# Performance work log

Hardware: AMD Instinct MI355X
Metric: run time of the kernel (lower is better)

Reference implementation:

```python
import jax, jax.numpy as jnp
import numpy as np

VOCAB = 32000
HID = 1024


def _gru_cell(Wih, Whh, bih, bhh, h, x):
    # PyTorch GRU gate order: r, z, n
    gx = Wih @ x + bih          # [3H]
    gh = Whh @ h + bhh          # [3H]
    H = h.shape[0]
    r = jax.nn.sigmoid(gx[:H] + gh[:H])
    z = jax.nn.sigmoid(gx[H:2 * H] + gh[H:2 * H])
    n = jnp.tanh(gx[2 * H:] + r * gh[2 * H:])
    return (1.0 - z) * n + z * h


def setup_inputs() -> dict:
    key = jax.random.key(0)
    ks = jax.random.split(key, 13)
    S = 512
    T = 512
    s = 1.0 / np.sqrt(HID)
    u = lambda k, shape: jax.random.uniform(k, shape, jnp.float32, -s, s)
    return {
        "inputs": jax.random.randint(ks[0], (S,), 0, VOCAB, jnp.int32),
        "targets": jax.random.randint(ks[1], (T,), 0, VOCAB, jnp.int32),
        "emb": jax.random.normal(ks[2], (VOCAB, HID), jnp.float32),
        "enc_Wih": u(ks[3], (3 * HID, HID)),
        "enc_Whh": u(ks[4], (3 * HID, HID)),
        "enc_bih": u(ks[5], (3 * HID,)),
        "enc_bhh": u(ks[6], (3 * HID,)),
        "dec_Wih": u(ks[7], (3 * HID, HID)),
        "dec_Whh": u(ks[8], (3 * HID, HID)),
        "dec_bih": u(ks[9], (3 * HID,)),
        "dec_bhh": u(ks[10], (3 * HID,)),
        "proj_W": u(ks[11], (VOCAB, HID)),
        "proj_b": u(ks[12], (VOCAB,)),
    }


def reference(inputs, targets, emb, enc_Wih, enc_Whh, enc_bih, enc_bhh,
              dec_Wih, dec_Whh, dec_bih, dec_bhh, proj_W, proj_b):
    # Encoder: scan GRU over embedded source tokens (batch=1, state [H])
    src_emb = emb[inputs]  # [S,H]
    h0 = jnp.zeros((HID,), src_emb.dtype)

    def enc_step(h, x):
        return _gru_cell(enc_Wih, enc_Whh, enc_bih, enc_bhh, h, x), None

    enc_state, _ = jax.lax.scan(enc_step, h0, src_emb)

    # Decoder: teacher forcing; input token at step i is 0 (start) then targets[i-1]
    dec_tokens = jnp.concatenate([jnp.zeros((1,), targets.dtype), targets[:-1]])
    dec_emb = emb[dec_tokens]  # [T,H]

    def dec_step(h, x):
        h_new = _gru_cell(dec_Wih, dec_Whh, dec_bih, dec_bhh, h, x)
        return h_new, h_new

    _, dec_hs = jax.lax.scan(dec_step, enc_state, dec_emb)  # [T,H]

    # Projection to vocab logits (single GEMM over all timesteps)
    logits = dec_hs @ proj_W.T + proj_b  # [T,V]
    return logits
```

## Files before the change

### kernel.cpp

```cpp
#include <hip/hip_runtime.h>
#include <cstdint>
#include <cstddef>

#define H 1024
#define SEQ 512
#define THREEH 3072
#define VOCABN 32000
#define NBLK 64
#define NWORK 192
#define HPB 16

#define HBIAS 2.0f
#define HVALID 0.5f

template <int CTRL>
__device__ __forceinline__ float dpp_add(float v) {
    return v + __int_as_float(__builtin_amdgcn_update_dpp(
        0, __float_as_int(v), CTRL, 0xF, 0xF, true));
}
__device__ __forceinline__ float row16_sum(float v) {
    v = dpp_add<0xB1>(v);
    v = dpp_add<0x4E>(v);
    v = dpp_add<0x124>(v);
    v = dpp_add<0x128>(v);
    return v;
}

__device__ void rnn_path(int blk, int tid, float* smem,
    const float* __restrict__ eWhh, const float* __restrict__ ebhh,
    const float* __restrict__ dWhh, const float* __restrict__ dbhh,
    const float* __restrict__ gxe, const float* __restrict__ gxd,
    float* __restrict__ enc_t, float* __restrict__ dec_t)
{
    const int wave = tid >> 6;
    const int lane = tid & 63;
    const int g = lane >> 4;
    const int p = lane & 15;
    const int i0 = blk * HPB;
    const int myidx = i0 + 4 * wave + g;

    float* hs0 = smem;
    float* hs1 = smem + H;

    float4 wreg[3][16];
    float br, bz, bn;
    float hown = 0.f;

    auto load_w = [&](const float* __restrict__ W, const float* __restrict__ b) {
        float ws[3];
#pragma unroll
        for (int gate = 0; gate < 3; ++gate) {
            const float* base = W + (size_t)(gate * H + myidx) * H + 64 * p;
            float s = 0.f;
#pragma unroll
            for (int k = 0; k < 16; ++k) {
                float4 w = *(const float4*)(base + 4 * ((k + p) & 15));
                wreg[gate][k] = w;
                s += w.x + w.y + w.z + w.w;
            }
            ws[gate] = s;
        }
        br = b[myidx]         - HBIAS * row16_sum(ws[0]);
        bz = b[H + myidx]     - HBIAS * row16_sum(ws[1]);
        bn = b[2 * H + myidx] - HBIAS * row16_sum(ws[2]);
    };

    load_w(eWhh, ebhh);

    for (int step = 0; step < 2 * SEQ; ++step) {
        const bool dec = step >= SEQ;
        const int t = dec ? step - SEQ : step;
        if (dec && t == 0) load_w(dWhh, dbhh);

        const float* gx = dec ? gxd : gxe;
        float* tb_out = (dec ? dec_t : enc_t) + (size_t)t * H;
        float* hb = (step & 1) ? hs1 : hs0;

        const float* gxp = gx + (size_t)t * THREEH + myidx;
        float gxr = gxp[0];
        float gxz = gxp[H];
        float gxn = gxp[2 * H];

        if (step == 0) {
            *(float4*)&hb[wave * 256 + lane * 4] =
                float4{HBIAS, HBIAS, HBIAS, HBIAS};
        } else {
            const float* tb_prev =
                (step <= SEQ) ? enc_t + (size_t)(step - 1) * H
                              : dec_t + (size_t)(step - SEQ - 1) * H;
            const unsigned long long* src =
                (const unsigned long long*)tb_prev + wave * 128 + lane * 2;
            union { unsigned long long u; float f[2]; } cv[2];
            for (;;) {
                cv[0].u = __hip_atomic_load(src,
                    __ATOMIC_RELAXED, __HIP_MEMORY_SCOPE_AGENT);
                cv[1].u = __hip_atomic_load(src + 1,
                    __ATOMIC_RELAXED, __HIP_MEMORY_SCOPE_AGENT);
                if ((cv[0].f[0] > HVALID) & (cv[0].f[1] > HVALID) &
                    (cv[1].f[0] > HVALID) & (cv[1].f[1] > HVALID)) break;
                __builtin_amdgcn_s_sleep(1);
            }
            *(float4*)&hb[wave * 256 + lane * 4] =
                float4{cv[0].f[0], cv[0].f[1], cv[1].f[0], cv[1].f[1]};
        }
        __syncthreads();

        float a0 = 0.f, a1 = 0.f, a2 = 0.f;
#pragma unroll
        for (int k = 0; k < 16; ++k) {
            float4 h = *(const float4*)&hb[64 * p + 4 * ((k + p) & 15)];
            float4 w0 = wreg[0][k], w1 = wreg[1][k], w2 = wreg[2][k];
            a0 += w0.x * h.x + w0.y * h.y + w0.z * h.z + w0.w * h.w;
            a1 += w1.x * h.x + w1.y * h.y + w1.z * h.z + w1.w * h.w;
            a2 += w2.x * h.x + w2.y * h.y + w2.z * h.z + w2.w * h.w;
        }
        float sr = row16_sum(a0);
        float sz = row16_sum(a1);
        float sn = row16_sum(a2);

        float rg = 1.f / (1.f + expf(-(gxr + sr + br)));
        float zg = 1.f / (1.f + expf(-(gxz + sz + bz)));
        float ng = tanhf(gxn + rg * (sn + bn));
        float hnew = (1.f - zg) * ng + zg * hown;
        hown = hnew;

        if (p == 0)
            __hip_atomic_store(tb_out + myidx, hnew + HBIAS,
                               __ATOMIC_RELAXED, __HIP_MEMORY_SCOPE_AGENT);
    }
}

template <int MODE>
__device__ void gemm_tile(const float* __restrict__ Abase,
                          int m0, int n0,
                          const float* __restrict__ W,
                          const float* __restrict__ bias,
                          float* __restrict__ C, int N,
                          float* __restrict__ sA, float* __restrict__ sB)
{
    const int tid = threadIdx.x;
    const int r = tid >> 2;
    const int c = tid & 3;
    const int tx = tid & 15;
    const int ty = tid >> 4;
    const int m = m0 + r;

    const float* Arow = Abase + (size_t)m * H;
    const float* Brow = W + (size_t)(n0 + r) * H;
    const float abias = (MODE == 2) ? HBIAS : 0.f;

    float acc[4][4] = {};
    for (int k0 = 0; k0 < H; k0 += 16) {
        float4 av = *(const float4*)(Arow + k0 + c * 4);
        float4 bv = *(const float4*)(Brow + k0 + c * 4);
        __syncthreads();
        sA[(c * 4 + 0) * 68 + r] = av.x - abias;
        sA[(c * 4 + 1) * 68 + r] = av.y - abias;
        sA[(c * 4 + 2) * 68 + r] = av.z - abias;
        sA[(c * 4 + 3) * 68 + r] = av.w - abias;
        sB[(c * 4 + 0) * 68 + r] = bv.x;
        sB[(c * 4 + 1) * 68 + r] = bv.y;
        sB[(c * 4 + 2) * 68 + r] = bv.z;
        sB[(c * 4 + 3) * 68 + r] = bv.w;
        __syncthreads();
#pragma unroll
        for (int kk = 0; kk < 16; ++kk) {
            float4 a = *(const float4*)&sA[kk * 68 + ty * 4];
            float4 b = *(const float4*)&sB[kk * 68 + tx * 4];
            float avv[4] = {a.x, a.y, a.z, a.w};
            float bvv[4] = {b.x, b.y, b.z, b.w};
#pragma unroll
            for (int i = 0; i < 4; ++i)
#pragma unroll
                for (int jj = 0; jj < 4; ++jj)
                    acc[i][jj] += avv[i] * bvv[jj];
        }
    }
    float4 bq = *(const float4*)(bias + n0 + tx * 4);
    float bb[4] = {bq.x, bq.y, bq.z, bq.w};
#pragma unroll
    for (int i = 0; i < 4; ++i) {
        float4 o;
        o.x = acc[i][0] + bb[0];
        o.y = acc[i][1] + bb[1];
        o.z = acc[i][2] + bb[2];
        o.w = acc[i][3] + bb[3];
        *(float4*)&C[(size_t)(m0 + ty * 4 + i) * N + n0 + tx * 4] = o;
    }
}

__device__ void worker_path(int wid, int tid, float* smem,
    const float* __restrict__ dec_t,
    const float* __restrict__ pW, const float* __restrict__ pb,
    float* __restrict__ out)
{
    float* sA = smem;
    float* sB = smem + 16 * 68;

    {
        float acc = 0.f;
        const size_t nlines = (size_t)VOCABN * H / 32;
        for (size_t i = (size_t)wid * 256 + tid; i < nlines;
             i += (size_t)NWORK * 256)
            acc += pW[i * 32];
        asm volatile("" :: "v"(acc));
    }

    int cur = -1;
    for (int tt = wid; tt < 8 * 500; tt += NWORK) {
        int mb = tt / 500, nb = tt % 500;
        if (mb != cur) {
            if (tid < 64) {
                const unsigned long long* src =
                    (const unsigned long long*)(dec_t + (size_t)(mb * 64 + 63) * H);
                for (;;) {
                    bool ok = true;
#pragma unroll
                    for (int m = 0; m < 8; ++m) {
                        union { unsigned long long u; float f[2]; } c;
                        c.u = __hip_atomic_load(src + tid + 64 * m,
                            __ATOMIC_RELAXED, __HIP_MEMORY_SCOPE_AGENT);
                        ok &= (c.f[0] > HVALID) & (c.f[1] > HVALID);
                    }
                    if (ok) break;
                    __builtin_amdgcn_s_sleep(64);
                }
            }
            __syncthreads();
            __builtin_amdgcn_fence(__ATOMIC_ACQUIRE, "agent");
            cur = mb;
        }
        gemm_tile<2>(dec_t, mb * 64, nb * 64, pW, pb, out, VOCABN, sA, sB);
    }
}

__global__ __launch_bounds__(256, 1) void fused_rnn(
    const float* __restrict__ eWhh, const float* __restrict__ ebhh,
    const float* __restrict__ dWhh, const float* __restrict__ dbhh,
    const float* __restrict__ gxe, const float* __restrict__ gxd,
    float* __restrict__ enc_t, float* __restrict__ dec_t,
    const float* __restrict__ pW, const float* __restrict__ pb,
    float* __restrict__ out)
{
    __shared__ float smem[2176];
    const int b = blockIdx.x;
    if (b < NBLK)
        rnn_path(b, threadIdx.x, smem, eWhh, ebhh, dWhh, dbhh,
                 gxe, gxd, enc_t, dec_t);
    else
        worker_path(b - NBLK, threadIdx.x, smem, dec_t, pW, pb, out);
}

__global__ __launch_bounds__(256, 2) void gemm_nt(
    const float* __restrict__ Abase,
    const int* __restrict__ toks0,
    const int* __restrict__ toks1,
    const int mode,
    const float* __restrict__ W,
    const float* __restrict__ bias,
    float* __restrict__ C, const int N)
{
    constexpr int TM = 64, TN = 64, TK = 16;
    __shared__ float As[TK][TM + 4];
    __shared__ float Bs[TK][TN + 4];
    const int tid = threadIdx.x;
    const int n0 = blockIdx.x * TN;
    const int m0 = blockIdx.y * TM;
    const int r = tid >> 2;
    const int c = tid & 3;
    const int tx = tid & 15;
    const int ty = tid >> 4;

    const int m = m0 + r;
    const float* Arow;
    if (mode == 0) Arow = Abase + (size_t)toks0[m] * H;
    else           Arow = Abase + (size_t)(m == 0 ? 0 : toks1[m - 1]) * H;
    const float* Brow = W + (size_t)(n0 + r) * H;

    float acc[4][4] = {};
    for (int k0 = 0; k0 < H; k0 += TK) {
        float4 av = *(const float4*)(Arow + k0 + c * 4);
        float4 bv = *(const float4*)(Brow + k0 + c * 4);
        __syncthreads();
        As[c * 4 + 0][r] = av.x; As[c * 4 + 1][r] = av.y;
        As[c * 4 + 2][r] = av.z; As[c * 4 + 3][r] = av.w;
        Bs[c * 4 + 0][r] = bv.x; Bs[c * 4 + 1][r] = bv.y;
        Bs[c * 4 + 2][r] = bv.z; Bs[c * 4 + 3][r] = bv.w;
        __syncthreads();
#pragma unroll
        for (int kk = 0; kk < TK; ++kk) {
            float4 a = *(const float4*)&As[kk][ty * 4];
            float4 b = *(const float4*)&Bs[kk][tx * 4];
            float avv[4] = {a.x, a.y, a.z, a.w};
            float bvv[4] = {b.x, b.y, b.z, b.w};
#pragma unroll
            for (int i = 0; i < 4; ++i)
#pragma unroll
                for (int jj = 0; jj < 4; ++jj)
                    acc[i][jj] += avv[i] * bvv[jj];
        }
    }

    float4 bq = *(const float4*)(bias + n0 + tx * 4);
    float bb[4] = {bq.x, bq.y, bq.z, bq.w};
#pragma unroll
    for (int i = 0; i < 4; ++i) {
        float4 o;
        o.x = acc[i][0] + bb[0];
        o.y = acc[i][1] + bb[1];
        o.z = acc[i][2] + bb[2];
        o.w = acc[i][3] + bb[3];
        *(float4*)&C[(size_t)(m0 + ty * 4 + i) * N + n0 + tx * 4] = o;
    }
}

extern "C" void kernel_launch(void* const* d_in, const int* in_sizes, int n_in,
                              void* d_out, int out_size, void* d_ws, size_t ws_size,
                              hipStream_t stream) {
    const int*   inputs  = (const int*)d_in[0];
    const int*   targets = (const int*)d_in[1];
    const float* emb     = (const float*)d_in[2];
    const float* eWih    = (const float*)d_in[3];
    const float* eWhh    = (const float*)d_in[4];
    const float* ebih    = (const float*)d_in[5];
    const float* ebhh    = (const float*)d_in[6];
    const float* dWih    = (const float*)d_in[7];
    const float* dWhh    = (const float*)d_in[8];
    const float* dbih    = (const float*)d_in[9];
    const float* dbhh    = (const float*)d_in[10];
    const float* pW      = (const float*)d_in[11];
    const float* pb      = (const float*)d_in[12];
    float* out = (float*)d_out;

    float* gxe   = (float*)d_ws;
    float* gxd   = gxe + (size_t)SEQ * THREEH;
    float* enc_t = gxd + (size_t)SEQ * THREEH;
    float* dec_t = enc_t + (size_t)SEQ * H;

    gemm_nt<<<dim3(THREEH / 64, SEQ / 64), 256, 0, stream>>>(
        emb, inputs, targets, 0, eWih, ebih, gxe, THREEH);
    gemm_nt<<<dim3(THREEH / 64, SEQ / 64), 256, 0, stream>>>(
        emb, inputs, targets, 1, dWih, dbih, gxd, THREEH);

    fused_rnn<<<NBLK + NWORK, 256, 0, stream>>>(
        eWhh, ebhh, dWhh, dbhh, gxe, gxd, enc_t, dec_t, pW, pb, out);
}
```

Before: 3.854 ms.

## Fuse input-projection GEMMs into persistent kernel and sync steps via per-block flags

Drops the two separate input-projection GEMM launches. The worker blocks of the persistent kernel now compute those projections and publish per-tile ready flags, and the recurrent blocks wait on those flags every 64 timesteps, so the projections overlap the start of the recurrence. The per-element validity polling of the hidden state is replaced by a per-step, per-block flag array: a wave polls 64 flags and then reads the hidden state without checking it. The aim is to remove launch gaps and serialization, but each step now pays an extra block barrier plus a flag write and read round trip on the critical path. The flags are never reset between calls, so a repeated call can see stale readiness.

```diff
diff --git a/kernel.cpp b/kernel.cpp
--- a/kernel.cpp
+++ b/kernel.cpp
@@ -30,7 +30,9 @@
     const float* __restrict__ eWhh, const float* __restrict__ ebhh,
     const float* __restrict__ dWhh, const float* __restrict__ dbhh,
     const float* __restrict__ gxe, const float* __restrict__ gxd,
-    float* __restrict__ enc_t, float* __restrict__ dec_t)
+    float* __restrict__ enc_t, float* __restrict__ dec_t,
+    float* __restrict__ tf,
+    const float* __restrict__ fe, const float* __restrict__ fd)
 {
     const int wave = tid >> 6;
     const int lane = tid & 63;
@@ -39,8 +41,7 @@
     const int i0 = blk * HPB;
     const int myidx = i0 + 4 * wave + g;
 
-    float* hs0 = smem;
-    float* hs1 = smem + H;
+    float* hb = smem;
 
     float4 wreg[3][16];
     float br, bz, bn;
@@ -72,18 +73,40 @@
         const int t = dec ? step - SEQ : step;
         if (dec && t == 0) load_w(dWhh, dbhh);
 
+        if ((t & 63) == 0) {
+            const float* fl = (dec ? fd : fe) + (t >> 6) * 64
+                              + (lane < 48 ? lane : 47);
+            for (;;) {
+                float f = __hip_atomic_load(fl,
+                    __ATOMIC_RELAXED, __HIP_MEMORY_SCOPE_AGENT);
+                if (__all(f > HVALID)) break;
+                __builtin_amdgcn_s_sleep(4);
+            }
+        }
+
         const float* gx = dec ? gxd : gxe;
         float* tb_out = (dec ? dec_t : enc_t) + (size_t)t * H;
-        float* hb = (step & 1) ? hs1 : hs0;
 
         const float* gxp = gx + (size_t)t * THREEH + myidx;
-        float gxr = gxp[0];
-        float gxz = gxp[H];
-        float gxn = gxp[2 * H];
+        float gxr = __hip_atomic_load(gxp,
+            __ATOMIC_RELAXED, __HIP_MEMORY_SCOPE_AGENT);
+        float gxz = __hip_atomic_load(gxp + H,
+            __ATOMIC_RELAXED, __HIP_MEMORY_SCOPE_AGENT);
+        float gxn = __hip_atomic_load(gxp + 2 * H,
+            __ATOMIC_RELAXED, __HIP_MEMORY_SCOPE_AGENT);
+
+        if (step > 0 && wave == 0) {
+            const float* fl = tf + (size_t)(step - 1) * 64 + lane;
+            for (;;) {
+                float f = __hip_atomic_load(fl,
+                    __ATOMIC_RELAXED, __HIP_MEMORY_SCOPE_AGENT);
+                if (__all(f > HVALID)) break;
+            }
+        }
+        __syncthreads();
 
         if (step == 0) {
-            *(float4*)&hb[wave * 256 + lane * 4] =
-                float4{HBIAS, HBIAS, HBIAS, HBIAS};
+            *(float4*)&hb[tid * 4] = float4{HBIAS, HBIAS, HBIAS, HBIAS};
         } else {
             const float* tb_prev =
                 (step <= SEQ) ? enc_t + (size_t)(step - 1) * H
@@ -91,15 +114,10 @@
             const unsigned long long* src =
                 (const unsigned long long*)tb_prev + wave * 128 + lane * 2;
             union { unsigned long long u; float f[2]; } cv[2];
-            for (;;) {
-                cv[0].u = __hip_atomic_load(src,
-                    __ATOMIC_RELAXED, __HIP_MEMORY_SCOPE_AGENT);
-                cv[1].u = __hip_atomic_load(src + 1,
-                    __ATOMIC_RELAXED, __HIP_MEMORY_SCOPE_AGENT);
-                if ((cv[0].f[0] > HVALID) & (cv[0].f[1] > HVALID) &
-                    (cv[1].f[0] > HVALID) & (cv[1].f[1] > HVALID)) break;
-                __builtin_amdgcn_s_sleep(1);
-            }
+            cv[0].u = __hip_atomic_load(src,
+                __ATOMIC_RELAXED, __HIP_MEMORY_SCOPE_AGENT);
+            cv[1].u = __hip_atomic_load(src + 1,
+                __ATOMIC_RELAXED, __HIP_MEMORY_SCOPE_AGENT);
             *(float4*)&hb[wave * 256 + lane * 4] =
                 float4{cv[0].f[0], cv[0].f[1], cv[1].f[0], cv[1].f[1]};
         }
@@ -127,11 +145,16 @@
         if (p == 0)
             __hip_atomic_store(tb_out + myidx, hnew + HBIAS,
                                __ATOMIC_RELAXED, __HIP_MEMORY_SCOPE_AGENT);
+        __syncthreads();
+        if (tid == 0)
+            __hip_atomic_store(tf + (size_t)step * 64 + blk, 1.0f,
+                               __ATOMIC_RELAXED, __HIP_MEMORY_SCOPE_AGENT);
     }
 }
 
 template <int MODE>
 __device__ void gemm_tile(const float* __restrict__ Abase,
+                          const int* __restrict__ toks,
                           int m0, int n0,
                           const float* __restrict__ W,
                           const float* __restrict__ bias,
@@ -145,7 +168,10 @@
     const int ty = tid >> 4;
     const int m = m0 + r;
 
-    const float* Arow = Abase + (size_t)m * H;
+    const float* Arow;
+    if (MODE == 0)      Arow = Abase + (size_t)toks[m] * H;
+    else if (MODE == 1) Arow = Abase + (size_t)(m == 0 ? 0 : toks[m - 1]) * H;
+    else                Arow = Abase + (size_t)m * H;
     const float* Brow = W + (size_t)(n0 + r) * H;
     const float abias = (MODE == 2) ? HBIAS : 0.f;
 
@@ -190,12 +216,39 @@
 }
 
 __device__ void worker_path(int wid, int tid, float* smem,
+    const float* __restrict__ emb,
+    const int* __restrict__ inputs, const int* __restrict__ targets,
+    const float* __restrict__ eWih, const float* __restrict__ ebih,
+    const float* __restrict__ dWih, const float* __restrict__ dbih,
+    float* __restrict__ gxe, float* __restrict__ gxd,
+    float* __restrict__ fe, float* __restrict__ fd,
     const float* __restrict__ dec_t,
     const float* __restrict__ pW, const float* __restrict__ pb,
     float* __restrict__ out)
 {
     float* sA = smem;
     float* sB = smem + 16 * 68;
+
+    for (int q = wid; q < 8 * 48; q += NWORK) {
+        int mb = q / 48, nb = q % 48;
+        gemm_tile<0>(emb, inputs, mb * 64, nb * 64, eWih, ebih,
+                     gxe, THREEH, sA, sB);
+        __threadfence();
+        __syncthreads();
+        if (tid == 0)
+            __hip_atomic_store(fe + mb * 64 + nb, 1.0f,
+                               __ATOMIC_RELAXED, __HIP_MEMORY_SCOPE_AGENT);
+    }
+    for (int q = wid; q < 8 * 48; q += NWORK) {
+        int mb = q / 48, nb = q % 48;
+        gemm_tile<1>(emb, targets, mb * 64, nb * 64, dWih, dbih,
+                     gxd, THREEH, sA, sB);
+        __threadfence();
+        __syncthreads();
+        if (tid == 0)
+            __hip_atomic_store(fd + mb * 64 + nb, 1.0f,
+                               __ATOMIC_RELAXED, __HIP_MEMORY_SCOPE_AGENT);
+    }
 
     {
         float acc = 0.f;
@@ -230,15 +283,21 @@
             __builtin_amdgcn_fence(__ATOMIC_ACQUIRE, "agent");
             cur = mb;
         }
-        gemm_tile<2>(dec_t, mb * 64, nb * 64, pW, pb, out, VOCABN, sA, sB);
+        gemm_tile<2>(dec_t, nullptr, mb * 64, nb * 64, pW, pb,
+                     out, VOCABN, sA, sB);
     }
 }
 
 __global__ __launch_bounds__(256, 1) void fused_rnn(
     const float* __restrict__ eWhh, const float* __restrict__ ebhh,
     const float* __restrict__ dWhh, const float* __restrict__ dbhh,
-    const float* __restrict__ gxe, const float* __restrict__ gxd,
+    float* __restrict__ gxe, float* __restrict__ gxd,
     float* __restrict__ enc_t, float* __restrict__ dec_t,
+    float* __restrict__ tf, float* __restrict__ fe, float* __restrict__ fd,
+    const float* __restrict__ emb,
+    const int* __restrict__ inputs, const int* __restrict__ targets,
+    const float* __restrict__ eWih, const float* __restrict__ ebih,
+    const float* __restrict__ dWih, const float* __restrict__ dbih,
     const float* __restrict__ pW, const float* __restrict__ pb,
     float* __restrict__ out)
 {
@@ -246,72 +305,11 @@
     const int b = blockIdx.x;
     if (b < NBLK)
         rnn_path(b, threadIdx.x, smem, eWhh, ebhh, dWhh, dbhh,
-                 gxe, gxd, enc_t, dec_t);
+                 gxe, gxd, enc_t, dec_t, tf, fe, fd);
     else
-        worker_path(b - NBLK, threadIdx.x, smem, dec_t, pW, pb, out);
-}
-
-__global__ __launch_bounds__(256, 2) void gemm_nt(
-    const float* __restrict__ Abase,
-    const int* __restrict__ toks0,
-    const int* __restrict__ toks1,
-    const int mode,
-    const float* __restrict__ W,
-    const float* __restrict__ bias,
-    float* __restrict__ C, const int N)
-{
-    constexpr int TM = 64, TN = 64, TK = 16;
-    __shared__ float As[TK][TM + 4];
-    __shared__ float Bs[TK][TN + 4];
-    const int tid = threadIdx.x;
-    const int n0 = blockIdx.x * TN;
-    const int m0 = blockIdx.y * TM;
-    const int r = tid >> 2;
-    const int c = tid & 3;
-    const int tx = tid & 15;
-    const int ty = tid >> 4;
-
-    const int m = m0 + r;
-    const float* Arow;
-    if (mode == 0) Arow = Abase + (size_t)toks0[m] * H;
-    else           Arow = Abase + (size_t)(m == 0 ? 0 : toks1[m - 1]) * H;
-    const float* Brow = W + (size_t)(n0 + r) * H;
-
-    float acc[4][4] = {};
-    for (int k0 = 0; k0 < H; k0 += TK) {
-        float4 av = *(const float4*)(Arow + k0 + c * 4);
-        float4 bv = *(const float4*)(Brow + k0 + c * 4);
-        __syncthreads();
-        As[c * 4 + 0][r] = av.x; As[c * 4 + 1][r] = av.y;
-        As[c * 4 + 2][r] = av.z; As[c * 4 + 3][r] = av.w;
-        Bs[c * 4 + 0][r] = bv.x; Bs[c * 4 + 1][r] = bv.y;
-        Bs[c * 4 + 2][r] = bv.z; Bs[c * 4 + 3][r] = bv.w;
-        __syncthreads();
-#pragma unroll
-        for (int kk = 0; kk < TK; ++kk) {
-            float4 a = *(const float4*)&As[kk][ty * 4];
-            float4 b = *(const float4*)&Bs[kk][tx * 4];
-            float avv[4] = {a.x, a.y, a.z, a.w};
-            float bvv[4] = {b.x, b.y, b.z, b.w};
-#pragma unroll
-            for (int i = 0; i < 4; ++i)
-#pragma unroll
-                for (int jj = 0; jj < 4; ++jj)
-                    acc[i][jj] += avv[i] * bvv[jj];
-        }
-    }
-
-    float4 bq = *(const float4*)(bias + n0 + tx * 4);
-    float bb[4] = {bq.x, bq.y, bq.z, bq.w};
-#pragma unroll
-    for (int i = 0; i < 4; ++i) {
-        float4 o;
-        o.x = acc[i][0] + bb[0];
-        o.y = acc[i][1] + bb[1];
-        o.z = acc[i][2] + bb[2];
-        o.w = acc[i][3] + bb[3];
-        *(float4*)&C[(size_t)(m0 + ty * 4 + i) * N + n0 + tx * 4] = o;
-    }
+        worker_path(b - NBLK, threadIdx.x, smem, emb, inputs, targets,
+                    eWih, ebih, dWih, dbih, gxe, gxd, fe, fd,
+                    dec_t, pW, pb, out);
 }
 
 extern "C" void kernel_launch(void* const* d_in, const int* in_sizes, int n_in,
@@ -336,12 +334,11 @@
     float* gxd   = gxe + (size_t)SEQ * THREEH;
     float* enc_t = gxd + (size_t)SEQ * THREEH;
     float* dec_t = enc_t + (size_t)SEQ * H;
-
-    gemm_nt<<<dim3(THREEH / 64, SEQ / 64), 256, 0, stream>>>(
-        emb, inputs, targets, 0, eWih, ebih, gxe, THREEH);
-    gemm_nt<<<dim3(THREEH / 64, SEQ / 64), 256, 0, stream>>>(
-        emb, inputs, targets, 1, dWih, dbih, gxd, THREEH);
+    float* tf    = dec_t + (size_t)SEQ * H;
+    float* fe    = tf + (size_t)2 * SEQ * 64;
+    float* fd    = fe + 8 * 64;
 
     fused_rnn<<<NBLK + NWORK, 256, 0, stream>>>(
-        eWhh, ebhh, dWhh, dbhh, gxe, gxd, enc_t, dec_t, pW, pb, out);
-}
+        eWhh, ebhh, dWhh, dbhh, gxe, gxd, enc_t, dec_t, tf, fe, fd,
+        emb, inputs, targets, eWih, ebih, dWih, dbih, pW, pb, out);
+}
```

Result: slower. 4.664 ms (+21.0%).
